# Optimization experiments

Hardware: AMD Instinct MI355X
Metric: run time of the kernel (lower is better)

Reference implementation:

```python
import jax, jax.numpy as jnp
import numpy as np

T, B, C, H, W = 128, 16, 4, 84, 84
NUM_ACTIONS, FEAT, HID = 18, 512, 256


def _conv(x, w, b, stride):
    # x: (N,C,H,W), w: (O,I,kh,kw)
    y = jax.lax.conv_general_dilated(
        x, w, window_strides=(stride, stride), padding='VALID',
        dimension_numbers=('NCHW', 'OIHW', 'NCHW'))
    return y + b[None, :, None, None]


def setup_inputs() -> dict:
    key = jax.random.key(0)
    ks = jax.random.split(key, 24)
    s = 0.05
    inp = {
        'obs_seq': jax.random.uniform(ks[0], (T, B, C, H, W), jnp.float32) * 255.0,
        'actions_seq': jax.random.randint(ks[1], (T, B), 0, NUM_ACTIONS),
        'episode_starts_seq': jax.random.randint(ks[2], (T, B), 0, 2).astype(jnp.float32),
        'h0': jnp.zeros((1, B, HID), jnp.float32),
        'c0': jnp.zeros((1, B, HID), jnp.float32),
        # NatureCNN params
        'conv1_w': jax.random.normal(ks[3], (32, C, 8, 8)) * s,
        'conv1_b': jnp.zeros((32,)),
        'conv2_w': jax.random.normal(ks[4], (64, 32, 4, 4)) * s,
        'conv2_b': jnp.zeros((64,)),
        'conv3_w': jax.random.normal(ks[5], (64, 64, 3, 3)) * s,
        'conv3_b': jnp.zeros((64,)),
        'fc_w': jax.random.normal(ks[6], (FEAT, 64 * 7 * 7)) * s,
        'fc_b': jnp.zeros((FEAT,)),
        # LSTM params (torch gate order i,f,g,o)
        'w_ih': jax.random.normal(ks[7], (4 * HID, FEAT)) * s,
        'w_hh': jax.random.normal(ks[8], (4 * HID, HID)) * s,
        'b_ih': jnp.zeros((4 * HID,)),
        'b_hh': jnp.zeros((4 * HID,)),
        # heads
        'actor_w': jax.random.normal(ks[9], (NUM_ACTIONS, HID)) * 0.01,
        'actor_b': jnp.zeros((NUM_ACTIONS,)),
        'critic_w': jax.random.normal(ks[10], (1, HID)) * s,
        'critic_b': jnp.zeros((1,)),
        'aux_w': jax.random.normal(ks[11], (1, FEAT)) * s,
        'aux_b': jnp.zeros((1,)),
    }
    return inp


def reference(obs_seq, actions_seq, episode_starts_seq, h0, c0,
              conv1_w, conv1_b, conv2_w, conv2_b, conv3_w, conv3_b,
              fc_w, fc_b, w_ih, w_hh, b_ih, b_hh,
              actor_w, actor_b, critic_w, critic_b, aux_w, aux_b):
    t, b = actions_seq.shape
    x = obs_seq.reshape(t * b, *obs_seq.shape[2:]) / 255.0
    x = jax.nn.relu(_conv(x, conv1_w, conv1_b, 4))   # (TB,32,20,20)
    x = jax.nn.relu(_conv(x, conv2_w, conv2_b, 2))   # (TB,64,9,9)
    x = jax.nn.relu(_conv(x, conv3_w, conv3_b, 1))   # (TB,64,7,7)
    feat = jax.nn.relu(x.reshape(t * b, -1) @ fc_w.T + fc_b)  # (TB,FEAT)

    aux_logits = (feat @ aux_w.T + aux_b).squeeze(-1).reshape(t, b)
    feat_seq = feat.reshape(t, b, -1)

    def step(carry, inp):
        h, c = carry
        x_t, s_t = inp
        keep = (1.0 - s_t)[:, None]
        h = h * keep
        c = c * keep
        gates = x_t @ w_ih.T + b_ih + h @ w_hh.T + b_hh  # (B,4H)
        i, f, g, o = jnp.split(gates, 4, axis=-1)
        c = jax.nn.sigmoid(f) * c + jax.nn.sigmoid(i) * jnp.tanh(g)
        h = jax.nn.sigmoid(o) * jnp.tanh(c)
        return (h, c), h

    _, out = jax.lax.scan(step, (h0[0], c0[0]), (feat_seq, episode_starts_seq))  # (T,B,HID)

    logits = out @ actor_w.T + actor_b
    logp = jax.nn.log_softmax(logits, axis=-1)
    log_probs = jnp.take_along_axis(logp, actions_seq[..., None], axis=-1).squeeze(-1)
    entropy = -jnp.sum(jnp.exp(logp) * logp, axis=-1)
    values = (out @ critic_w.T + critic_b).squeeze(-1)
    return log_probs, entropy, values, aux_logits
```

## Files before the change

kernel.cpp:

```cpp
#include <hip/hip_runtime.h>
#include <hip/hip_bf16.h>
#include <cstddef>

typedef __attribute__((ext_vector_type(8))) short bf16x8;
typedef __attribute__((ext_vector_type(4))) float f32x4;

static constexpr size_t OFF_X1B   = 0;
static constexpr size_t OFF_X2B   = 52428800;
static constexpr size_t OFF_X3B   = 73662464;
static constexpr size_t OFF_FEATB = 86507520;
static constexpr size_t OFF_W2B   = 88604672;
static constexpr size_t OFF_W3B   = 88670208;
static constexpr size_t OFF_FCWB  = 88743936;
static constexpr size_t OFF_WIHB  = 91955200;
static constexpr size_t OFF_FEAT  = 93003776;
static constexpr size_t OFF_GX    = 97198080;
static constexpr size_t OFF_HSEQ  = 105586688;
static constexpr size_t OFF_W1B   = 108732416;
static constexpr size_t OFF_WHHB  = 108748800;
static constexpr size_t OFF_ORDB  = 109273088;
static constexpr size_t OFF_ORDT0 = 109281280;
static constexpr size_t OFF_ORDLEN= 109289472;
static constexpr size_t OFF_NSEG  = 109297664;

__device__ __forceinline__ float sigmoidf_(float x) {
  return 1.0f / (1.0f + __expf(-x));
}

__global__ __launch_bounds__(256) void prep_kernel(
    const float* __restrict__ c1w, const float* __restrict__ c2w,
    const float* __restrict__ c3w, const float* __restrict__ fcw,
    const float* __restrict__ wih, const float* __restrict__ whh,
    __hip_bfloat16* __restrict__ w1b,
    __hip_bfloat16* __restrict__ w2b, __hip_bfloat16* __restrict__ w3b,
    __hip_bfloat16* __restrict__ fcwb, __hip_bfloat16* __restrict__ wihb,
    __hip_bfloat16* __restrict__ whhb) {
  int i = blockIdx.x * 256 + threadIdx.x;
  if (i < 32768) {
    int o = i >> 9, k = i & 511;
    int pos = k >> 5, ci = k & 31;
    int ky = pos >> 2, kx = pos & 3;
    w2b[i] = __float2bfloat16(c2w[o * 512 + ci * 16 + ky * 4 + kx]);
  } else if (i < 69632) {
    int j = i - 32768;
    int o = j / 576, k = j - o * 576;
    int pos = k >> 6, ci = k & 63;
    int ky = pos / 3, kx = pos - ky * 3;
    w3b[j] = __float2bfloat16(c3w[o * 576 + ci * 9 + ky * 3 + kx]);
  } else if (i < 1675264) {
    int j = i - 69632;
    int o = j / 3136, k = j - o * 3136;
    int sp = k >> 6, ci = k & 63;
    fcwb[j] = __float2bfloat16(fcw[o * 3136 + ci * 49 + sp]);
  } else if (i < 2199552) {
    int j = i - 1675264;
    wihb[j] = __float2bfloat16(wih[j]);
  } else if (i < 2461696) {
    int j = i - 2199552;
    whhb[j] = __float2bfloat16(whh[j]);
  } else if (i < 2469888) {
    int j = i - 2461696;
    int oc = j >> 8, k = j & 255;
    int ky = k >> 5, rem = k & 31;
    int ci = rem >> 3, kx = rem & 7;
    w1b[j] = __float2bfloat16(c1w[oc * 256 + ci * 64 + ky * 8 + kx] * (1.0f / 255.0f));
  }
}

__global__ __launch_bounds__(256) void plan_kernel(
    const float* __restrict__ starts, int* __restrict__ ord_b,
    int* __restrict__ ord_t0, int* __restrict__ ord_len,
    int* __restrict__ nseg_out) {
  __shared__ int s_t0[2048];
  __shared__ int s_len[2048];
  __shared__ int cnt[16];
  __shared__ int hist[132];
  __shared__ int off[132];
  const int tid = threadIdx.x;
  if (tid < 16) {
    int b = tid, c = 0;
    for (int t = 0; t < 128; ++t) {
      float s = starts[t * 16 + b];
      if (t == 0 || s != 0.0f) {
        if (c > 0) s_len[b * 128 + c - 1] = t - s_t0[b * 128 + c - 1];
        s_t0[b * 128 + c] = t;
        ++c;
      }
    }
    s_len[b * 128 + c - 1] = 128 - s_t0[b * 128 + c - 1];
    cnt[b] = c;
  }
  if (tid < 132) hist[tid] = 0;
  __syncthreads();
  for (int idx = tid; idx < 2048; idx += 256) {
    int b = idx >> 7, i = idx & 127;
    if (i < cnt[b]) atomicAdd(&hist[s_len[idx]], 1);
  }
  __syncthreads();
  if (tid == 0) {
    int running = 0;
    for (int L = 128; L >= 1; --L) { off[L] = running; running += hist[L]; }
    *nseg_out = running;
  }
  __syncthreads();
  for (int idx = tid; idx < 2048; idx += 256) {
    int b = idx >> 7, i = idx & 127;
    if (i < cnt[b]) {
      int len = s_len[idx];
      int pos = atomicAdd(&off[len], 1);
      ord_b[pos] = b;
      ord_t0[pos] = s_t0[idx];
      ord_len[pos] = len;
    }
  }
}

__global__ __launch_bounds__(256) void conv1_mfma(
    const float* __restrict__ obs, const __hip_bfloat16* __restrict__ w1b,
    const float* __restrict__ b1, __hip_bfloat16* __restrict__ x1b) {
  constexpr int LDK = 40;
  __shared__ __align__(16) __hip_bfloat16 As[128 * LDK];
  __shared__ __align__(16) __hip_bfloat16 Ws[32 * LDK];
  const int tid = threadIdx.x;
  const int m0 = blockIdx.x * 128;
  const int l = tid & 63;
  const int wv = tid >> 6;
  const int lane16 = l & 15;
  const int quad = l >> 4;
  const int m_base = wv * 32;

  f32x4 acc[2][2] = {};

  const float* arow[2];
  int arw[2], acp[2];
#pragma unroll
  for (int c = 0; c < 2; ++c) {
    const int id = tid + c * 256;
    const int row = id >> 2, cpos = id & 3;
    arw[c] = row; acp[c] = cpos;
    const int m = m0 + row;
    const int n = m / 400, sp = m - n * 400;
    const int oy = sp / 20, ox = sp - oy * 20;
    arow[c] = obs + (size_t)n * 28224 + cpos * 7056 + (oy * 4) * 84 + ox * 4;
  }
  const int wrow = tid >> 2, wcp = tid & 3;
  const __hip_bfloat16* wsrc = w1b + wrow * 256 + wcp * 8;

  for (int s = 0; s < 8; ++s) {
    float4 p[2], q[2];
#pragma unroll
    for (int c = 0; c < 2; ++c) {
      const float* r = arow[c] + s * 84;
      p[c] = *(const float4*)r;
      q[c] = *(const float4*)(r + 4);
    }
    uint4 wval;
    if (tid < 128) wval = *(const uint4*)(wsrc + s * 32);
    __syncthreads();
#pragma unroll
    for (int c = 0; c < 2; ++c) {
      __hip_bfloat16* d = &As[arw[c] * LDK + acp[c] * 8];
      d[0] = __float2bfloat16(p[c].x); d[1] = __float2bfloat16(p[c].y);
      d[2] = __float2bfloat16(p[c].z); d[3] = __float2bfloat16(p[c].w);
      d[4] = __float2bfloat16(q[c].x); d[5] = __float2bfloat16(q[c].y);
      d[6] = __float2bfloat16(q[c].z); d[7] = __float2bfloat16(q[c].w);
    }
    if (tid < 128) *(uint4*)&Ws[wrow * LDK + wcp * 8] = wval;
    __syncthreads();
    const bf16x8 a0 = *(const bf16x8*)&As[(m_base + lane16) * LDK + quad * 8];
    const bf16x8 a1 = *(const bf16x8*)&As[(m_base + 16 + lane16) * LDK + quad * 8];
#pragma unroll
    for (int nf = 0; nf < 2; ++nf) {
      const bf16x8 b = *(const bf16x8*)&Ws[(nf * 16 + lane16) * LDK + quad * 8];
      acc[0][nf] = __builtin_amdgcn_mfma_f32_16x16x32_bf16(a0, b, acc[0][nf], 0, 0, 0);
      acc[1][nf] = __builtin_amdgcn_mfma_f32_16x16x32_bf16(a1, b, acc[1][nf], 0, 0, 0);
    }
  }
#pragma unroll
  for (int nf = 0; nf < 2; ++nf) {
    const int col = nf * 16 + lane16;
    const float bb = b1[col];
#pragma unroll
    for (int mf = 0; mf < 2; ++mf) {
#pragma unroll
      for (int r = 0; r < 4; ++r) {
        const int row = m0 + m_base + mf * 16 + quad * 4 + r;
        const float v = fmaxf(acc[mf][nf][r] + bb, 0.f);
        x1b[(size_t)row * 32 + col] = __float2bfloat16(v);
      }
    }
  }
}

template<int BM, int MODE>
__global__ __launch_bounds__(256) void gemm_mfma(
    const __hip_bfloat16* __restrict__ Abase,
    const __hip_bfloat16* __restrict__ Wb,
    const float* __restrict__ bias1, const float* __restrict__ bias2,
    float* __restrict__ Cf, __hip_bfloat16* __restrict__ Cb,
    const int M, const int N, const int K, const int relu) {
  constexpr int LDK = 40;
  __shared__ __align__(16) __hip_bfloat16 As[BM * LDK];
  __shared__ __align__(16) __hip_bfloat16 Ws[64 * LDK];
  const int tid = threadIdx.x;
  const int m0 = blockIdx.y * BM;
  const int n0 = blockIdx.x * 64;
  const int l = tid & 63;
  const int wv = tid >> 6;
  const int lane16 = l & 15;
  const int quad = l >> 4;
  constexpr int NF = (BM == 128) ? 4 : 2;
  const int m_base = (BM == 128) ? wv * 32 : (wv & 1) * 32;
  const int n_base = (BM == 128) ? 0 : (wv >> 1) * 32;
  constexpr int NCA = (BM == 128) ? 2 : 1;

  f32x4 acc[2][NF] = {};

  const __hip_bfloat16* arow[NCA];
  int acp[NCA];
#pragma unroll
  for (int c = 0; c < NCA; ++c) {
    const int id = tid + c * 256;
    const int row = id >> 2, cpos = id & 3;
    const int m = m0 + row;
    acp[c] = cpos;
    if (MODE == 0) {
      arow[c] = Abase + (size_t)m * K + cpos * 8;
    } else if (MODE == 1) {
      const int n = m / 81, sp = m - n * 81;
      const int oy = sp / 9, ox = sp - oy * 9;
      arow[c] = Abase + ((n * 20 + oy * 2) * 20 + ox * 2) * 32 + cpos * 8;
    } else {
      const int n = m / 49, sp = m - n * 49;
      const int oy = sp / 7, ox = sp - oy * 7;
      arow[c] = Abase + ((n * 9 + oy) * 9 + ox) * 64 + cpos * 8;
    }
  }
  const int wrow = tid >> 2, wcp = tid & 3;
  const __hip_bfloat16* wsrc = Wb + (size_t)(n0 + wrow) * K + wcp * 8;

  const int ksteps = K >> 5;
  for (int s = 0; s < ksteps; ++s) {
    uint4 av[NCA];
#pragma unroll
    for (int c = 0; c < NCA; ++c) {
      const __hip_bfloat16* p;
      if (MODE == 0) {
        p = arow[c] + s * 32;
      } else if (MODE == 1) {
        p = arow[c] + ((s >> 2) * 20 + (s & 3)) * 32;
      } else {
        const int pos = s >> 1;
        const int ky = pos / 3, kx = pos - ky * 3;
        p = arow[c] + (ky * 9 + kx) * 64 + (s & 1) * 32;
      }
      av[c] = *(const uint4*)p;
    }
    const uint4 wval = *(const uint4*)(wsrc + s * 32);
    __syncthreads();
#pragma unroll
    for (int c = 0; c < NCA; ++c) {
      const int row = (tid + c * 256) >> 2;
      *(uint4*)&As[row * LDK + acp[c] * 8] = av[c];
    }
    *(uint4*)&Ws[wrow * LDK + wcp * 8] = wval;
    __syncthreads();
    const bf16x8 a0 = *(const bf16x8*)&As[(m_base + lane16) * LDK + quad * 8];
    const bf16x8 a1 = *(const bf16x8*)&As[(m_base + 16 + lane16) * LDK + quad * 8];
#pragma unroll
    for (int nf = 0; nf < NF; ++nf) {
      const bf16x8 b = *(const bf16x8*)&Ws[(n_base + nf * 16 + lane16) * LDK + quad * 8];
      acc[0][nf] = __builtin_amdgcn_mfma_f32_16x16x32_bf16(a0, b, acc[0][nf], 0, 0, 0);
      acc[1][nf] = __builtin_amdgcn_mfma_f32_16x16x32_bf16(a1, b, acc[1][nf], 0, 0, 0);
    }
  }
#pragma unroll
  for (int nf = 0; nf < NF; ++nf) {
    const int col = n0 + n_base + nf * 16 + lane16;
    float bb = bias1[col];
    if (bias2) bb += bias2[col];
#pragma unroll
    for (int mf = 0; mf < 2; ++mf) {
#pragma unroll
      for (int r = 0; r < 4; ++r) {
        const int row = m0 + m_base + mf * 16 + quad * 4 + r;
        float v = acc[mf][nf][r] + bb;
        if (relu) v = fmaxf(v, 0.f);
        if (Cf) Cf[(size_t)row * N + col] = v;
        if (Cb) Cb[(size_t)row * N + col] = __float2bfloat16(v);
      }
    }
  }
}

__global__ __launch_bounds__(1024, 4) void lstm_mfma(
    const float* __restrict__ gx, const __hip_bfloat16* __restrict__ whhb,
    const float* __restrict__ starts, const float* __restrict__ h0,
    const float* __restrict__ c0, const int* __restrict__ ord_b,
    const int* __restrict__ ord_t0, const int* __restrict__ ord_len,
    const int* __restrict__ nseg_p, float* __restrict__ hseq) {
  constexpr int LDH = 264;
  constexpr int PS  = 1028;
  __shared__ __align__(16) __hip_bfloat16 h_lds[16 * LDH];
  __shared__ __align__(16) float pre[16 * PS];
  __shared__ int sg_b[16], sg_t0[16], sg_len[16];
  const int g = blockIdx.x;
  const int nseg = *nseg_p;
  if (g * 16 >= nseg) return;
  const int tid = threadIdx.x;
  const int wv = tid >> 6;
  const int l = tid & 63;
  const int lane16 = l & 15, quad = l >> 4;
  if (tid < 16) {
    const int s = g * 16 + tid;
    sg_b[tid] = (s < nseg) ? ord_b[s] : 0;
    sg_t0[tid] = (s < nseg) ? ord_t0[s] : 0;
    sg_len[tid] = (s < nseg) ? ord_len[s] : 0;
  }
  __syncthreads();
  bf16x8 bfrag[4][8];
#pragma unroll
  for (int nt = 0; nt < 4; ++nt)
#pragma unroll
    for (int ks = 0; ks < 8; ++ks)
      bfrag[nt][ks] = *(const bf16x8*)&whhb[
          (size_t)(wv * 64 + nt * 16 + lane16) * 256 + ks * 32 + quad * 8];
  const int m_own = wv;
  const int u = l * 4;
  const int b_own = sg_b[m_own];
  const int t0_own = sg_t0[m_own];
  const int len_own = sg_len[m_own];
  float4 c_reg = make_float4(0.f, 0.f, 0.f, 0.f);
  {
    float4 hv = make_float4(0.f, 0.f, 0.f, 0.f);
    if (len_own > 0 && t0_own == 0) {
      const float keep = 1.0f - starts[b_own];
      const float4 h4 = *(const float4*)&h0[b_own * 256 + u];
      const float4 c4 = *(const float4*)&c0[b_own * 256 + u];
      hv = make_float4(h4.x * keep, h4.y * keep, h4.z * keep, h4.w * keep);
      c_reg = make_float4(c4.x * keep, c4.y * keep, c4.z * keep, c4.w * keep);
    }
    __hip_bfloat16* hd = &h_lds[m_own * LDH + u];
    hd[0] = __float2bfloat16(hv.x); hd[1] = __float2bfloat16(hv.y);
    hd[2] = __float2bfloat16(hv.z); hd[3] = __float2bfloat16(hv.w);
  }
  const int maxlen = sg_len[0];
  for (int tt = 0; tt < maxlen; ++tt) {
    __syncthreads();
    const bool act = tt < len_own;
    const int t = t0_own + tt;
    const size_t gbase = act ? ((size_t)(t * 16 + b_own) * 1024 + u) : 0;
    const float4 g0 = *(const float4*)&gx[gbase];
    const float4 g1 = *(const float4*)&gx[gbase + 256];
    const float4 g2 = *(const float4*)&gx[gbase + 512];
    const float4 g3 = *(const float4*)&gx[gbase + 768];
    bf16x8 afr[8];
#pragma unroll
    for (int ks = 0; ks < 8; ++ks)
      afr[ks] = *(const bf16x8*)&h_lds[lane16 * LDH + ks * 32 + quad * 8];
    f32x4 acc[4] = {};
#pragma unroll
    for (int nt = 0; nt < 4; ++nt)
#pragma unroll
      for (int ks = 0; ks < 8; ++ks)
        acc[nt] = __builtin_amdgcn_mfma_f32_16x16x32_bf16(
            afr[ks], bfrag[nt][ks], acc[nt], 0, 0, 0);
#pragma unroll
    for (int nt = 0; nt < 4; ++nt)
#pragma unroll
      for (int r = 0; r < 4; ++r)
        pre[(quad * 4 + r) * PS + wv * 64 + nt * 16 + lane16] = acc[nt][r];
    __syncthreads();
    if (act) {
      const float4 p0 = *(const float4*)&pre[m_own * PS + u];
      const float4 p1 = *(const float4*)&pre[m_own * PS + u + 256];
      const float4 p2 = *(const float4*)&pre[m_own * PS + u + 512];
      const float4 p3 = *(const float4*)&pre[m_own * PS + u + 768];
      const float i0 = sigmoidf_(p0.x + g0.x), i1 = sigmoidf_(p0.y + g0.y),
                  i2 = sigmoidf_(p0.z + g0.z), i3 = sigmoidf_(p0.w + g0.w);
      const float f0 = sigmoidf_(p1.x + g1.x), f1 = sigmoidf_(p1.y + g1.y),
                  f2 = sigmoidf_(p1.z + g1.z), f3 = sigmoidf_(p1.w + g1.w);
      const float q0 = tanhf(p2.x + g2.x), q1 = tanhf(p2.y + g2.y),
                  q2 = tanhf(p2.z + g2.z), q3 = tanhf(p2.w + g2.w);
      const float o0 = sigmoidf_(p3.x + g3.x), o1 = sigmoidf_(p3.y + g3.y),
                  o2 = sigmoidf_(p3.z + g3.z), o3 = sigmoidf_(p3.w + g3.w);
      c_reg.x = fmaf(f0, c_reg.x, i0 * q0);
      c_reg.y = fmaf(f1, c_reg.y, i1 * q1);
      c_reg.z = fmaf(f2, c_reg.z, i2 * q2);
      c_reg.w = fmaf(f3, c_reg.w, i3 * q3);
      const float4 h4 = make_float4(o0 * tanhf(c_reg.x), o1 * tanhf(c_reg.y),
                                    o2 * tanhf(c_reg.z), o3 * tanhf(c_reg.w));
      __hip_bfloat16* hd = &h_lds[m_own * LDH + u];
      hd[0] = __float2bfloat16(h4.x); hd[1] = __float2bfloat16(h4.y);
      hd[2] = __float2bfloat16(h4.z); hd[3] = __float2bfloat16(h4.w);
      *(float4*)&hseq[(size_t)(t * 16 + b_own) * 256 + u] = h4;
    }
  }
}

__global__ __launch_bounds__(256) void aux_kernel(
    const float* __restrict__ feat, const float* __restrict__ aux_w,
    const float* __restrict__ aux_b, float* __restrict__ outp) {
  const int tb = blockIdx.x;
  const int tid = threadIdx.x;
  __shared__ float red[256];
  const float* f = feat + (size_t)tb * 512;
  red[tid] = f[tid] * aux_w[tid] + f[tid + 256] * aux_w[tid + 256];
  __syncthreads();
  for (int s = 128; s > 0; s >>= 1) {
    if (tid < s) red[tid] += red[tid + s];
    __syncthreads();
  }
  if (tid == 0) outp[6144 + tb] = red[0] + aux_b[0];
}

__global__ __launch_bounds__(64) void heads_kernel(
    const float* __restrict__ hseq, const int* __restrict__ actions,
    const float* __restrict__ actor_w, const float* __restrict__ actor_b,
    const float* __restrict__ critic_w, const float* __restrict__ critic_b,
    float* __restrict__ outp) {
  const int tb = blockIdx.x;
  const int tid = threadIdx.x;
  __shared__ float h[256];
  __shared__ float lg[32];
#pragma unroll
  for (int i = 0; i < 4; ++i) h[tid + 64 * i] = hseq[(size_t)tb * 256 + tid + 64 * i];
  __syncthreads();
  if (tid < 18) {
    float a = actor_b[tid];
    const float* w = actor_w + tid * 256;
    for (int kk = 0; kk < 256; ++kk) a = fmaf(h[kk], w[kk], a);
    lg[tid] = a;
  } else if (tid == 18) {
    float v = critic_b[0];
    for (int kk = 0; kk < 256; ++kk) v = fmaf(h[kk], critic_w[kk], v);
    lg[18] = v;
  }
  __syncthreads();
  if (tid == 0) {
    float m = -1e30f;
    for (int i = 0; i < 18; ++i) m = fmaxf(m, lg[i]);
    float se = 0.f;
    for (int i = 0; i < 18; ++i) se += expf(lg[i] - m);
    const float lse = logf(se);
    float ent = 0.f;
    for (int i = 0; i < 18; ++i) {
      const float lp = lg[i] - m - lse;
      ent -= expf(lp) * lp;
    }
    const int a = actions[tb];
    outp[tb] = lg[a] - m - lse;
    outp[2048 + tb] = ent;
    outp[4096 + tb] = lg[18];
  }
}

extern "C" void kernel_launch(void* const* d_in, const int* in_sizes, int n_in,
                              void* d_out, int out_size, void* d_ws, size_t ws_size,
                              hipStream_t stream) {
  const float* obs     = (const float*)d_in[0];
  const int*   actions = (const int*)d_in[1];
  const float* starts  = (const float*)d_in[2];
  const float* h0      = (const float*)d_in[3];
  const float* c0      = (const float*)d_in[4];
  const float* c1w     = (const float*)d_in[5];
  const float* c1b     = (const float*)d_in[6];
  const float* c2w     = (const float*)d_in[7];
  const float* c2b     = (const float*)d_in[8];
  const float* c3w     = (const float*)d_in[9];
  const float* c3b     = (const float*)d_in[10];
  const float* fcw     = (const float*)d_in[11];
  const float* fcb     = (const float*)d_in[12];
  const float* wih     = (const float*)d_in[13];
  const float* whh     = (const float*)d_in[14];
  const float* bih     = (const float*)d_in[15];
  const float* bhh     = (const float*)d_in[16];
  const float* aw      = (const float*)d_in[17];
  const float* ab      = (const float*)d_in[18];
  const float* cw      = (const float*)d_in[19];
  const float* cb      = (const float*)d_in[20];
  const float* auxw    = (const float*)d_in[21];
  const float* auxb    = (const float*)d_in[22];

  char* ws = (char*)d_ws;
  __hip_bfloat16* x1b   = (__hip_bfloat16*)(ws + OFF_X1B);
  __hip_bfloat16* x2b   = (__hip_bfloat16*)(ws + OFF_X2B);
  __hip_bfloat16* x3b   = (__hip_bfloat16*)(ws + OFF_X3B);
  __hip_bfloat16* featb = (__hip_bfloat16*)(ws + OFF_FEATB);
  __hip_bfloat16* w2b   = (__hip_bfloat16*)(ws + OFF_W2B);
  __hip_bfloat16* w3b   = (__hip_bfloat16*)(ws + OFF_W3B);
  __hip_bfloat16* fcwb  = (__hip_bfloat16*)(ws + OFF_FCWB);
  __hip_bfloat16* wihb  = (__hip_bfloat16*)(ws + OFF_WIHB);
  __hip_bfloat16* w1b   = (__hip_bfloat16*)(ws + OFF_W1B);
  __hip_bfloat16* whhb  = (__hip_bfloat16*)(ws + OFF_WHHB);
  float* feat = (float*)(ws + OFF_FEAT);
  float* gx   = (float*)(ws + OFF_GX);
  float* hseq = (float*)(ws + OFF_HSEQ);
  int* ord_b   = (int*)(ws + OFF_ORDB);
  int* ord_t0  = (int*)(ws + OFF_ORDT0);
  int* ord_len = (int*)(ws + OFF_ORDLEN);
  int* nseg    = (int*)(ws + OFF_NSEG);
  float* outp = (float*)d_out;

  prep_kernel<<<9648, 256, 0, stream>>>(c1w, c2w, c3w, fcw, wih, whh,
                                        w1b, w2b, w3b, fcwb, wihb, whhb);
  plan_kernel<<<1, 256, 0, stream>>>(starts, ord_b, ord_t0, ord_len, nseg);
  conv1_mfma<<<6400, 256, 0, stream>>>(obs, w1b, c1b, x1b);
  gemm_mfma<128, 1><<<dim3(1, 1296), 256, 0, stream>>>(
      x1b, w2b, c2b, nullptr, nullptr, x2b, 165888, 64, 512, 1);
  gemm_mfma<128, 2><<<dim3(1, 784), 256, 0, stream>>>(
      x2b, w3b, c3b, nullptr, nullptr, x3b, 100352, 64, 576, 1);
  gemm_mfma<64, 0><<<dim3(8, 32), 256, 0, stream>>>(
      x3b, fcwb, fcb, nullptr, feat, featb, 2048, 512, 3136, 1);
  gemm_mfma<64, 0><<<dim3(16, 32), 256, 0, stream>>>(
      featb, wihb, bih, bhh, gx, nullptr, 2048, 1024, 512, 0);
  aux_kernel<<<2048, 256, 0, stream>>>(feat, auxw, auxb, outp);
  lstm_mfma<<<128, 1024, 0, stream>>>(gx, whhb, starts, h0, c0,
                                      ord_b, ord_t0, ord_len, nseg, hseq);
  heads_kernel<<<2048, 64, 0, stream>>>(hseq, actions, aw, ab, cw, cb, outp);
}
```

Before: 798.5 us.

## Cut LSTM register pressure, use fast tanh, and parallelize heads with wave reductions

The LSTM kernel now keeps only half of the W_hh fragments in registers and streams the other half from global memory on each step. This lowers register pressure at 1024 threads per block. The gx loads move after the MFMA phase so they happen only for active rows. tanhf is replaced by an exp-based approximation, which shortens the serial recurrence but slightly changes numerics. The heads kernel is rewritten so each wavefront handles one timestep with vectorized loads and shuffle reductions, instead of a single thread doing serial 256-long dot products.

Measured after the change: 773.1 us. -3.2%, faster.

```diff
diff --git a/kernel.cpp b/kernel.cpp
--- a/kernel.cpp
+++ b/kernel.cpp
@@ -25,6 +25,9 @@
 
 __device__ __forceinline__ float sigmoidf_(float x) {
   return 1.0f / (1.0f + __expf(-x));
+}
+__device__ __forceinline__ float tanhf_(float x) {
+  return 1.0f - 2.0f / (__expf(2.0f * x) + 1.0f);
 }
 
 __global__ __launch_bounds__(256) void prep_kernel(
@@ -318,13 +321,16 @@
     sg_len[tid] = (s < nseg) ? ord_len[s] : 0;
   }
   __syncthreads();
-  bf16x8 bfrag[4][8];
-#pragma unroll
-  for (int nt = 0; nt < 4; ++nt)
+  bf16x8 bfrag[2][8];
+#pragma unroll
+  for (int nt = 0; nt < 2; ++nt)
 #pragma unroll
     for (int ks = 0; ks < 8; ++ks)
       bfrag[nt][ks] = *(const bf16x8*)&whhb[
           (size_t)(wv * 64 + nt * 16 + lane16) * 256 + ks * 32 + quad * 8];
+  const __hip_bfloat16* bs2 = &whhb[(size_t)(wv * 64 + 32 + lane16) * 256 + quad * 8];
+  const __hip_bfloat16* bs3 = &whhb[(size_t)(wv * 64 + 48 + lane16) * 256 + quad * 8];
+
   const int m_own = wv;
   const int u = l * 4;
   const int b_own = sg_b[m_own];
@@ -347,31 +353,30 @@
   const int maxlen = sg_len[0];
   for (int tt = 0; tt < maxlen; ++tt) {
     __syncthreads();
-    const bool act = tt < len_own;
-    const int t = t0_own + tt;
-    const size_t gbase = act ? ((size_t)(t * 16 + b_own) * 1024 + u) : 0;
-    const float4 g0 = *(const float4*)&gx[gbase];
-    const float4 g1 = *(const float4*)&gx[gbase + 256];
-    const float4 g2 = *(const float4*)&gx[gbase + 512];
-    const float4 g3 = *(const float4*)&gx[gbase + 768];
-    bf16x8 afr[8];
-#pragma unroll
-    for (int ks = 0; ks < 8; ++ks)
-      afr[ks] = *(const bf16x8*)&h_lds[lane16 * LDH + ks * 32 + quad * 8];
     f32x4 acc[4] = {};
 #pragma unroll
-    for (int nt = 0; nt < 4; ++nt)
-#pragma unroll
-      for (int ks = 0; ks < 8; ++ks)
-        acc[nt] = __builtin_amdgcn_mfma_f32_16x16x32_bf16(
-            afr[ks], bfrag[nt][ks], acc[nt], 0, 0, 0);
+    for (int ks = 0; ks < 8; ++ks) {
+      const bf16x8 b2 = *(const bf16x8*)(bs2 + ks * 32);
+      const bf16x8 b3 = *(const bf16x8*)(bs3 + ks * 32);
+      const bf16x8 a = *(const bf16x8*)&h_lds[lane16 * LDH + ks * 32 + quad * 8];
+      acc[0] = __builtin_amdgcn_mfma_f32_16x16x32_bf16(a, bfrag[0][ks], acc[0], 0, 0, 0);
+      acc[1] = __builtin_amdgcn_mfma_f32_16x16x32_bf16(a, bfrag[1][ks], acc[1], 0, 0, 0);
+      acc[2] = __builtin_amdgcn_mfma_f32_16x16x32_bf16(a, b2, acc[2], 0, 0, 0);
+      acc[3] = __builtin_amdgcn_mfma_f32_16x16x32_bf16(a, b3, acc[3], 0, 0, 0);
+    }
 #pragma unroll
     for (int nt = 0; nt < 4; ++nt)
 #pragma unroll
       for (int r = 0; r < 4; ++r)
         pre[(quad * 4 + r) * PS + wv * 64 + nt * 16 + lane16] = acc[nt][r];
     __syncthreads();
-    if (act) {
+    if (tt < len_own) {
+      const int t = t0_own + tt;
+      const size_t gbase = (size_t)(t * 16 + b_own) * 1024 + u;
+      const float4 g0 = *(const float4*)&gx[gbase];
+      const float4 g1 = *(const float4*)&gx[gbase + 256];
+      const float4 g2 = *(const float4*)&gx[gbase + 512];
+      const float4 g3 = *(const float4*)&gx[gbase + 768];
       const float4 p0 = *(const float4*)&pre[m_own * PS + u];
       const float4 p1 = *(const float4*)&pre[m_own * PS + u + 256];
       const float4 p2 = *(const float4*)&pre[m_own * PS + u + 512];
@@ -380,16 +385,16 @@
                   i2 = sigmoidf_(p0.z + g0.z), i3 = sigmoidf_(p0.w + g0.w);
       const float f0 = sigmoidf_(p1.x + g1.x), f1 = sigmoidf_(p1.y + g1.y),
                   f2 = sigmoidf_(p1.z + g1.z), f3 = sigmoidf_(p1.w + g1.w);
-      const float q0 = tanhf(p2.x + g2.x), q1 = tanhf(p2.y + g2.y),
-                  q2 = tanhf(p2.z + g2.z), q3 = tanhf(p2.w + g2.w);
+      const float q0 = tanhf_(p2.x + g2.x), q1 = tanhf_(p2.y + g2.y),
+                  q2 = tanhf_(p2.z + g2.z), q3 = tanhf_(p2.w + g2.w);
       const float o0 = sigmoidf_(p3.x + g3.x), o1 = sigmoidf_(p3.y + g3.y),
                   o2 = sigmoidf_(p3.z + g3.z), o3 = sigmoidf_(p3.w + g3.w);
       c_reg.x = fmaf(f0, c_reg.x, i0 * q0);
       c_reg.y = fmaf(f1, c_reg.y, i1 * q1);
       c_reg.z = fmaf(f2, c_reg.z, i2 * q2);
       c_reg.w = fmaf(f3, c_reg.w, i3 * q3);
-      const float4 h4 = make_float4(o0 * tanhf(c_reg.x), o1 * tanhf(c_reg.y),
-                                    o2 * tanhf(c_reg.z), o3 * tanhf(c_reg.w));
+      const float4 h4 = make_float4(o0 * tanhf_(c_reg.x), o1 * tanhf_(c_reg.y),
+                                    o2 * tanhf_(c_reg.z), o3 * tanhf_(c_reg.w));
       __hip_bfloat16* hd = &h_lds[m_own * LDH + u];
       hd[0] = __float2bfloat16(h4.x); hd[1] = __float2bfloat16(h4.y);
       hd[2] = __float2bfloat16(h4.z); hd[3] = __float2bfloat16(h4.w);
@@ -414,44 +419,52 @@
   if (tid == 0) outp[6144 + tb] = red[0] + aux_b[0];
 }
 
-__global__ __launch_bounds__(64) void heads_kernel(
+__global__ __launch_bounds__(256) void heads_kernel(
     const float* __restrict__ hseq, const int* __restrict__ actions,
     const float* __restrict__ actor_w, const float* __restrict__ actor_b,
     const float* __restrict__ critic_w, const float* __restrict__ critic_b,
     float* __restrict__ outp) {
-  const int tb = blockIdx.x;
   const int tid = threadIdx.x;
-  __shared__ float h[256];
-  __shared__ float lg[32];
-#pragma unroll
-  for (int i = 0; i < 4; ++i) h[tid + 64 * i] = hseq[(size_t)tb * 256 + tid + 64 * i];
-  __syncthreads();
-  if (tid < 18) {
-    float a = actor_b[tid];
-    const float* w = actor_w + tid * 256;
-    for (int kk = 0; kk < 256; ++kk) a = fmaf(h[kk], w[kk], a);
-    lg[tid] = a;
-  } else if (tid == 18) {
-    float v = critic_b[0];
-    for (int kk = 0; kk < 256; ++kk) v = fmaf(h[kk], critic_w[kk], v);
-    lg[18] = v;
-  }
-  __syncthreads();
-  if (tid == 0) {
-    float m = -1e30f;
-    for (int i = 0; i < 18; ++i) m = fmaxf(m, lg[i]);
-    float se = 0.f;
-    for (int i = 0; i < 18; ++i) se += expf(lg[i] - m);
-    const float lse = logf(se);
-    float ent = 0.f;
-    for (int i = 0; i < 18; ++i) {
-      const float lp = lg[i] - m - lse;
-      ent -= expf(lp) * lp;
-    }
+  const int wv = tid >> 6, l = tid & 63;
+  const int tb = blockIdx.x * 4 + wv;
+  const float4 h4 = *(const float4*)&hseq[(size_t)tb * 256 + l * 4];
+  float part[19];
+#pragma unroll
+  for (int o = 0; o < 18; ++o) {
+    const float4 w = *(const float4*)&actor_w[o * 256 + l * 4];
+    part[o] = h4.x * w.x + h4.y * w.y + h4.z * w.z + h4.w * w.w;
+  }
+  {
+    const float4 w = *(const float4*)&critic_w[l * 4];
+    part[18] = h4.x * w.x + h4.y * w.y + h4.z * w.z + h4.w * w.w;
+  }
+#pragma unroll
+  for (int off = 32; off > 0; off >>= 1) {
+#pragma unroll
+    for (int o = 0; o < 19; ++o) part[o] += __shfl_xor(part[o], off);
+  }
+  float lg[18];
+  float m = -1e30f;
+#pragma unroll
+  for (int o = 0; o < 18; ++o) {
+    lg[o] = part[o] + actor_b[o];
+    m = fmaxf(m, lg[o]);
+  }
+  float se = 0.f;
+#pragma unroll
+  for (int o = 0; o < 18; ++o) se += __expf(lg[o] - m);
+  const float lse = __logf(se);
+  float ent = 0.f;
+#pragma unroll
+  for (int o = 0; o < 18; ++o) {
+    const float lp = lg[o] - m - lse;
+    ent -= __expf(lp) * lp;
+  }
+  if (l == 0) {
     const int a = actions[tb];
     outp[tb] = lg[a] - m - lse;
     outp[2048 + tb] = ent;
-    outp[4096 + tb] = lg[18];
+    outp[4096 + tb] = part[18] + critic_b[0];
   }
 }
 
@@ -517,5 +530,5 @@
   aux_kernel<<<2048, 256, 0, stream>>>(feat, auxw, auxb, outp);
   lstm_mfma<<<128, 1024, 0, stream>>>(gx, whhb, starts, h0, c0,
                                       ord_b, ord_t0, ord_len, nseg, hseq);
-  heads_kernel<<<2048, 64, 0, stream>>>(hseq, actions, aw, ab, cw, cb, outp);
-}
+  heads_kernel<<<512, 256, 0, stream>>>(hseq, actions, aw, ab, cw, cb, outp);
+}
```
